# Kernel optimization log

Measured on AMD Instinct MI355X. Metric: run time of the kernel, lower is better.

The kernel has to match this reference:

```python
import jax, jax.numpy as jnp
import numpy as np

B, DIM, H, W = 4, 512, 64, 64
HEADS = 8
MAX_FREQ = 10000.0


def _rope_cos_sin(h, w, head_dim, dtype):
    # 2D RoPE: first quarter of half_dim uses row position, second quarter uses col position
    half = head_dim // 2
    quarter = half // 2
    pos_h = jnp.arange(h, dtype=dtype)
    pos_w = jnp.arange(w, dtype=dtype)
    gh, gw = jnp.meshgrid(pos_h, pos_w, indexing='ij')
    pos = jnp.stack([gh.ravel(), gw.ravel()], axis=-1)  # [N, 2]
    freqs = 1.0 / (MAX_FREQ ** (jnp.arange(quarter, dtype=dtype) / quarter))  # [quarter]
    ang_x = pos[:, 0:1] * freqs  # [N, quarter]
    ang_y = pos[:, 1:2] * freqs  # [N, quarter]
    cos = jnp.concatenate([jnp.cos(ang_x), jnp.cos(ang_y)], axis=-1)  # [N, half]
    sin = jnp.concatenate([jnp.sin(ang_x), jnp.sin(ang_y)], axis=-1)  # [N, half]
    return cos, sin


def _apply_rope(x, cos, sin):
    # x: [B, heads, N, head_dim]; cos/sin: [N, head_dim//2]
    d = x.shape[-1] // 2
    x1, x2 = x[..., :d], x[..., d:]
    return jnp.concatenate([x1 * cos - x2 * sin, x1 * sin + x2 * cos], axis=-1)


def setup_inputs() -> dict:
    key = jax.random.key(0)
    kx, kq, kp = jax.random.split(key, 3)
    x = jax.random.normal(kx, (B, DIM, H, W), dtype=jnp.float32)
    w_qkv = jax.random.normal(kq, (3 * DIM, DIM), dtype=jnp.float32) * (DIM ** -0.5)
    w_proj = jax.random.normal(kp, (DIM, DIM), dtype=jnp.float32) * (DIM ** -0.5)
    return {"x": x, "w_qkv": w_qkv, "w_proj": w_proj}


def reference(x, w_qkv, w_proj):
    Bb, C, Hh, Ww = x.shape
    heads = HEADS
    hd = C // heads
    N = Hh * Ww
    # 1x1 conv (bias-free) == channel-wise linear
    qkv = jnp.einsum('bchw,oc->bohw', x, w_qkv)  # [B, 3C, H, W]
    qkv = qkv.reshape(Bb, 3, heads, hd, Hh, Ww).transpose(1, 0, 2, 4, 5, 3)  # [3, B, heads, H, W, hd]
    q = qkv[0].reshape(Bb, heads, N, hd)
    k = qkv[1].reshape(Bb, heads, N, hd)
    v = qkv[2].reshape(Bb, heads, N, hd)
    cos, sin = _rope_cos_sin(Hh, Ww, hd, x.dtype)
    q = _apply_rope(q, cos, sin)
    k = _apply_rope(k, cos, sin)
    scale = hd ** -0.5
    attn = jax.nn.softmax(jnp.einsum('bhnd,bhmd->bhnm', q, k) * scale, axis=-1)  # [B, heads, N, N]
    out = jnp.einsum('bhnm,bhmd->bhnd', attn, v)  # [B, heads, N, hd]
    out = out.reshape(Bb, heads, Hh, Ww, hd).transpose(0, 1, 4, 2, 3).reshape(Bb, C, Hh, Ww)
    return jnp.einsum('bchw,oc->bohw', out, w_proj)
```

## Files before the change

### kernel.cpp

```cpp
#include <hip/hip_runtime.h>
#include <math.h>

#define B_    4
#define CDIM  512
#define HEADS 8
#define HD    64
#define NN    4096
#define QSZ   ((size_t)B_*HEADS*NN*HD)
#define SCALE_Q 0.18033688011112042f

typedef __attribute__((ext_vector_type(8))) short short8;
typedef __attribute__((ext_vector_type(4))) float f32x4;
typedef __attribute__((ext_vector_type(16))) float f32x16;
union U4S8 { uint4 u; short8 s; };

__device__ inline unsigned pk(float a, float b) {
    unsigned ua = __float_as_uint(a), ub = __float_as_uint(b);
    ua += 0x7FFFu + ((ua >> 16) & 1u);
    ub += 0x7FFFu + ((ub >> 16) & 1u);
    return (ua >> 16) | (ub & 0xFFFF0000u);
}
__device__ inline unsigned short bf16_1(float a) {
    unsigned ua = __float_as_uint(a);
    ua += 0x7FFFu + ((ua >> 16) & 1u);
    return (unsigned short)(ua >> 16);
}
__device__ inline unsigned cvtpk(float a, float b) {
    unsigned r;
    asm("v_cvt_pk_bf16_f32 %0, %1, %2" : "=v"(r) : "v"(a), "v"(b));
    return r;
}

__device__ inline void load_lds16(const unsigned short* g, unsigned short* l) {
    __builtin_amdgcn_global_load_lds(
        (const __attribute__((address_space(1))) unsigned int*)g,
        (__attribute__((address_space(3))) unsigned int*)l, 16, 0, 0);
}

__global__ void conv_w_kernel(const float* __restrict__ wq, const float* __restrict__ wp,
                              unsigned short* __restrict__ wqb, unsigned short* __restrict__ wpb) {
    int id = blockIdx.x * 256 + threadIdx.x;
    const float* src; unsigned short* dst; size_t off; float sc = 1.0f;
    if (id < 98304) { src = wq; dst = wqb; off = (size_t)id * 8; if (off < 262144) sc = SCALE_Q; }
    else            { src = wp; dst = wpb; off = (size_t)(id - 98304) * 8; }
    float4 a = *(const float4*)(src + off);
    float4 b = *(const float4*)(src + off + 4);
    uint4 u;
    u.x = pk(a.x * sc, a.y * sc); u.y = pk(a.z * sc, a.w * sc);
    u.z = pk(b.x * sc, b.y * sc); u.w = pk(b.z * sc, b.w * sc);
    *(uint4*)(dst + off) = u;
}

__global__ void rope_table_kernel(float* __restrict__ ct, float* __restrict__ st) {
    int id = blockIdx.x * 256 + threadIdx.x;
    int j = id >> 12, n = id & 4095;
    int i = j & 15;
    float pos = (j < 16) ? (float)(n >> 6) : (float)(n & 63);
    float freq = exp2f(-(float)i * 0.8304820237218406f);
    float ang = pos * freq;
    ct[id] = cosf(ang);
    st[id] = sinf(ang);
}

__global__ __launch_bounds__(256) void transpose_x_kernel(
        const float* __restrict__ x, unsigned short* __restrict__ xt) {
    __shared__ unsigned short T[64 * 72];
    int t = threadIdx.x;
    int b = blockIdx.z, c0 = blockIdx.y * 64, n0 = blockIdx.x * 64;
    const float* xb = x + ((size_t)b * CDIM + c0) * NN + n0;
    int crow = t >> 2, nseg = t & 3;
#pragma unroll
    for (int g = 0; g < 4; ++g) {
        float4 f = *(const float4*)(xb + (size_t)crow * NN + nseg * 16 + g * 4);
        int nb = nseg * 16 + g * 4;
        T[(nb + 0) * 72 + crow] = bf16_1(f.x);
        T[(nb + 1) * 72 + crow] = bf16_1(f.y);
        T[(nb + 2) * 72 + crow] = bf16_1(f.z);
        T[(nb + 3) * 72 + crow] = bf16_1(f.w);
    }
    __syncthreads();
    unsigned short* xo = xt + ((size_t)b * NN + n0) * CDIM + c0;
    int nrow = t >> 2, cseg = t & 3;
    uint4 u0 = *(uint4*)(T + nrow * 72 + cseg * 16);
    uint4 u1 = *(uint4*)(T + nrow * 72 + cseg * 16 + 8);
    *(uint4*)(xo + (size_t)nrow * CDIM + cseg * 16)     = u0;
    *(uint4*)(xo + (size_t)nrow * CDIM + cseg * 16 + 8) = u1;
}

__global__ __launch_bounds__(256, 2) void qkv_mfma_kernel(
        const unsigned short* __restrict__ xt, const unsigned short* __restrict__ wq,
        unsigned short* __restrict__ qbf, unsigned short* __restrict__ kbf,
        unsigned short* __restrict__ vt,
        const float* __restrict__ ct, const float* __restrict__ st) {
    __shared__ unsigned short smem[8192];
    int t = threadIdx.x;
    int lane = t & 63, w = t >> 6;
    int qlo = lane & 15, quad = lane >> 4;
    int b = blockIdx.z, o0 = blockIdx.y * 128, n0 = blockIdx.x * 128;
    const unsigned short* xb = xt + (size_t)b * NN * CDIM;
    int row = t >> 2, seg = t & 3;
    int wn = (w & 1) * 64, wo = (w >> 1) * 64;

    f32x4 acc[4][4];
#pragma unroll
    for (int i = 0; i < 4; ++i)
#pragma unroll
        for (int j = 0; j < 4; ++j) acc[i][j] = f32x4{0.f, 0.f, 0.f, 0.f};

    for (int k0 = 0; k0 < 512; k0 += 32) {
        __syncthreads();
        load_lds16(xb + (size_t)(n0 + row) * 512 + k0 + seg * 8,        smem + t * 8);
        load_lds16(xb + (size_t)(n0 + 64 + row) * 512 + k0 + seg * 8,   smem + 2048 + t * 8);
        load_lds16(wq + (size_t)(o0 + row) * 512 + k0 + seg * 8,        smem + 4096 + t * 8);
        load_lds16(wq + (size_t)(o0 + 64 + row) * 512 + k0 + seg * 8,   smem + 6144 + t * 8);
        __syncthreads();
        U4S8 af[4], bf[4];
#pragma unroll
        for (int mt = 0; mt < 4; ++mt)
            af[mt].u = *(const uint4*)(smem + (wn + 16 * mt + qlo) * 32 + quad * 8);
#pragma unroll
        for (int nt = 0; nt < 4; ++nt)
            bf[nt].u = *(const uint4*)(smem + 4096 + (wo + 16 * nt + qlo) * 32 + quad * 8);
#pragma unroll
        for (int mt = 0; mt < 4; ++mt)
#pragma unroll
            for (int nt = 0; nt < 4; ++nt)
                acc[mt][nt] = __builtin_amdgcn_mfma_f32_16x16x32_bf16(
                    af[mt].s, bf[nt].s, acc[mt][nt], 0, 0, 0);
    }

    int og = o0 + wo;
    int s = og >> 9;
    int h = (og & 511) >> 6;
    int bh = b * HEADS + h;
    if (s < 2) {
        unsigned short* dst = (s ? kbf : qbf) + (size_t)bh * NN * HD;
#pragma unroll
        for (int mt = 0; mt < 4; ++mt) {
            int nbase = n0 + wn + 16 * mt + 4 * quad;
#pragma unroll
            for (int ntp = 0; ntp < 2; ++ntp) {
                int j = 16 * ntp + qlo;
                float4 c4 = *(const float4*)(ct + (size_t)j * NN + nbase);
                float4 s4 = *(const float4*)(st + (size_t)j * NN + nbase);
                float cc[4] = {c4.x, c4.y, c4.z, c4.w};
                float ss[4] = {s4.x, s4.y, s4.z, s4.w};
#pragma unroll
                for (int r = 0; r < 4; ++r) {
                    float x1 = acc[mt][ntp][r], x2 = acc[mt][ntp + 2][r];
                    size_t base = (size_t)(nbase + r) * HD;
                    dst[base + j]      = bf16_1(x1 * cc[r] - x2 * ss[r]);
                    dst[base + j + 32] = bf16_1(x1 * ss[r] + x2 * cc[r]);
                }
            }
        }
    } else {
        unsigned short* dst = vt + (size_t)bh * HD * NN;
#pragma unroll
        for (int mt = 0; mt < 4; ++mt)
#pragma unroll
            for (int nt = 0; nt < 4; ++nt) {
                int d = 16 * nt + qlo;
                int n = n0 + wn + 16 * mt + 4 * quad;
                uint2 u;
                u.x = pk(acc[mt][nt][0], acc[mt][nt][1]);
                u.y = pk(acc[mt][nt][2], acc[mt][nt][3]);
                *(uint2*)(dst + (size_t)d * NN + n) = u;
            }
    }
}

#define EXP_GRP(Sv, MTQ, KSL, PA)                                        \
    {                                                                    \
        float p0 = __builtin_amdgcn_exp2f(Sv[8 * (KSL) + 0]);            \
        float p1 = __builtin_amdgcn_exp2f(Sv[8 * (KSL) + 1]);            \
        float p2 = __builtin_amdgcn_exp2f(Sv[8 * (KSL) + 2]);            \
        float p3 = __builtin_amdgcn_exp2f(Sv[8 * (KSL) + 3]);            \
        float p4 = __builtin_amdgcn_exp2f(Sv[8 * (KSL) + 4]);            \
        float p5 = __builtin_amdgcn_exp2f(Sv[8 * (KSL) + 5]);            \
        float p6 = __builtin_amdgcn_exp2f(Sv[8 * (KSL) + 6]);            \
        float p7 = __builtin_amdgcn_exp2f(Sv[8 * (KSL) + 7]);            \
        Lsum[MTQ] += ((p0 + p1) + (p2 + p3)) + ((p4 + p5) + (p6 + p7));  \
        PA.u.x = cvtpk(p0, p1); PA.u.y = cvtpk(p2, p3);                  \
        PA.u.z = cvtpk(p4, p5); PA.u.w = cvtpk(p6, p7);                  \
    }

#define MFMA32(A, B, C) __builtin_amdgcn_mfma_f32_32x32x16_bf16((A), (B), (C), 0, 0, 0)

#define HALF_STEP_PF(SCONS, SPROD, KAC, KAN, KN_B, KN_H, VB_B, V_H)                      \
    {                                                                                    \
        U4S8 vb0, vb1, vb2, vb3;                                                         \
        vb0.u = *(const uint4*)((VB_B) + l31 * 144 + (V_H) * 64 + 16 * h);               \
        vb1.u = *(const uint4*)((VB_B) + (32 + l31) * 144 + (V_H) * 64 + 16 * h);        \
        vb2.u = *(const uint4*)((VB_B) + l31 * 144 + (V_H) * 64 + 32 + 16 * h);          \
        vb3.u = *(const uint4*)((VB_B) + (32 + l31) * 144 + (V_H) * 64 + 32 + 16 * h);   \
        KAN[0].u = *(const uint4*)((KN_B) + ((KN_H) * 32 + l31) * 144 + 16 * h);         \
        KAN[1].u = *(const uint4*)((KN_B) + ((KN_H) * 32 + l31) * 144 + 32 + 16 * h);    \
        KAN[2].u = *(const uint4*)((KN_B) + ((KN_H) * 32 + l31) * 144 + 64 + 16 * h);    \
        KAN[3].u = *(const uint4*)((KN_B) + ((KN_H) * 32 + l31) * 144 + 96 + 16 * h);    \
        U4S8 pa[2][2];                                                                   \
        SPROD[0] = MFMA32(KAC[0].s, qf[0][0].s, Zv);                                     \
        SPROD[1] = MFMA32(KAC[0].s, qf[1][0].s, Zv);                                     \
        EXP_GRP(SCONS[0], 0, 0, pa[0][0]);                                               \
        SPROD[0] = MFMA32(KAC[1].s, qf[0][1].s, SPROD[0]);                               \
        SPROD[1] = MFMA32(KAC[1].s, qf[1][1].s, SPROD[1]);                               \
        EXP_GRP(SCONS[0], 0, 1, pa[1][0]);                                               \
        SPROD[0] = MFMA32(KAC[2].s, qf[0][2].s, SPROD[0]);                               \
        SPROD[1] = MFMA32(KAC[2].s, qf[1][2].s, SPROD[1]);                               \
        EXP_GRP(SCONS[1], 1, 0, pa[0][1]);                                               \
        SPROD[0] = MFMA32(KAC[3].s, qf[0][3].s, SPROD[0]);                               \
        SPROD[1] = MFMA32(KAC[3].s, qf[1][3].s, SPROD[1]);                               \
        EXP_GRP(SCONS[1], 1, 1, pa[1][1]);                                               \
        O[0][0] = MFMA32(pa[0][0].s, vb0.s, O[0][0]);                                    \
        O[1][0] = MFMA32(pa[0][1].s, vb0.s, O[1][0]);                                    \
        O[0][1] = MFMA32(pa[0][0].s, vb1.s, O[0][1]);                                    \
        O[1][1] = MFMA32(pa[0][1].s, vb1.s, O[1][1]);                                    \
        O[0][0] = MFMA32(pa[1][0].s, vb2.s, O[0][0]);                                    \
        O[1][0] = MFMA32(pa[1][1].s, vb2.s, O[1][0]);                                    \
        O[0][1] = MFMA32(pa[1][0].s, vb3.s, O[0][1]);                                    \
        O[1][1] = MFMA32(pa[1][1].s, vb3.s, O[1][1]);                                    \
    }

__global__ __launch_bounds__(256, 2) void attn_kernel(
        const unsigned short* __restrict__ qbf, const unsigned short* __restrict__ kbf,
        const unsigned short* __restrict__ vt, unsigned short* __restrict__ aot) {
    __shared__ unsigned char smem[55296];
    int t = threadIdx.x;
    int lane = t & 63, w = t >> 6;
    int l31 = lane & 31, h = lane >> 5;
    int bb = blockIdx.z, hh = blockIdx.y;
    int bh = bb * HEADS + hh;
    int n0w = blockIdx.x * 256 + w * 64;

    U4S8 qf[2][4];
    const unsigned short* qg = qbf + ((size_t)bh * NN + n0w) * HD;
#pragma unroll
    for (int mtq = 0; mtq < 2; ++mtq)
#pragma unroll
        for (int ks = 0; ks < 4; ++ks)
            qf[mtq][ks].u = *(const uint4*)(qg + (size_t)(32 * mtq + l31) * 64 + 16 * ks + 8 * h);

    f32x16 Zv;
#pragma unroll
    for (int i = 0; i < 16; ++i) Zv[i] = 0.f;

    f32x16 O[2][2];
#pragma unroll
    for (int mtq = 0; mtq < 2; ++mtq)
#pragma unroll
        for (int ntd = 0; ntd < 2; ++ntd) O[mtq][ntd] = Zv;
    float Lsum[2] = {0.f, 0.f};

    const uint4* kg = (const uint4*)kbf + (size_t)bh * NN * 8;
    const uint4* vg = (const uint4*)vt  + (size_t)bh * 64 * 512;

    int rr0 = t >> 3, s8 = t & 7;
    int voff = 32 * (s8 >> 1) + 8 * (s8 & 1);

    const uint4* kp0 = kg + rr0 * 8 + s8;
    const uint4* kp1 = kg + (32 + rr0) * 8 + s8;
    const uint4* vp0 = vg + rr0 * 512 + s8;
    const uint4* vp1 = vg + (32 + rr0) * 512 + s8;

    unsigned char* kd0 = smem + rr0 * 144 + s8 * 16;
    unsigned char* kd1 = smem + (32 + rr0) * 144 + s8 * 16;
    unsigned char* vd0 = smem + 9216 + rr0 * 144 + voff;
    unsigned char* vd1 = smem + 9216 + (32 + rr0) * 144 + voff;

    uint4 kr0, kr1, vr0, vr1;
#pragma unroll
    for (int pt = 0; pt < 2; ++pt) {
        kr0 = kp0[0]; kr1 = kp1[0]; vr0 = vp0[0]; vr1 = vp1[0];
        kp0 += 512; kp1 += 512; vp0 += 8; vp1 += 8;
        int bo = pt * 18432;
        *(uint4*)(kd0 + bo) = kr0;
        *(uint4*)(kd1 + bo) = kr1;
        *(uint2*)(vd0 + bo)      = make_uint2(vr0.x, vr0.y);
        *(uint2*)(vd0 + bo + 16) = make_uint2(vr0.z, vr0.w);
        *(uint2*)(vd1 + bo)      = make_uint2(vr1.x, vr1.y);
        *(uint2*)(vd1 + bo + 16) = make_uint2(vr1.z, vr1.w);
    }
    kr0 = kp0[0]; kr1 = kp1[0]; vr0 = vp0[0]; vr1 = vp1[0];
    kp0 += 512; kp1 += 512; vp0 += 8; vp1 += 8;
    __syncthreads();

    f32x16 SA[2], SB[2];
    U4S8 kaA[4], kaB[4];
    {
        U4S8 ka0, ka1, ka2, ka3;
        ka0.u = *(const uint4*)(smem + l31 * 144 + 16 * h);
        ka1.u = *(const uint4*)(smem + l31 * 144 + 32 + 16 * h);
        ka2.u = *(const uint4*)(smem + l31 * 144 + 64 + 16 * h);
        ka3.u = *(const uint4*)(smem + l31 * 144 + 96 + 16 * h);
        kaA[0].u = *(const uint4*)(smem + (32 + l31) * 144 + 16 * h);
        kaA[1].u = *(const uint4*)(smem + (32 + l31) * 144 + 32 + 16 * h);
        kaA[2].u = *(const uint4*)(smem + (32 + l31) * 144 + 64 + 16 * h);
        kaA[3].u = *(const uint4*)(smem + (32 + l31) * 144 + 96 + 16 * h);
        SB[0] = MFMA32(ka0.s, qf[0][0].s, Zv);
        SB[1] = MFMA32(ka0.s, qf[1][0].s, Zv);
        SB[0] = MFMA32(ka1.s, qf[0][1].s, SB[0]);
        SB[1] = MFMA32(ka1.s, qf[1][1].s, SB[1]);
        SB[0] = MFMA32(ka2.s, qf[0][2].s, SB[0]);
        SB[1] = MFMA32(ka2.s, qf[1][2].s, SB[1]);
        SB[0] = MFMA32(ka3.s, qf[0][3].s, SB[0]);
        SB[1] = MFMA32(ka3.s, qf[1][3].s, SB[1]);
    }

    int b0 = 0, b1 = 18432, b2 = 36864;
    for (int c = 0; c < 63; ++c) {
        *(uint4*)(kd0 + b2) = kr0;
        *(uint4*)(kd1 + b2) = kr1;
        *(uint2*)(vd0 + b2)      = make_uint2(vr0.x, vr0.y);
        *(uint2*)(vd0 + b2 + 16) = make_uint2(vr0.z, vr0.w);
        *(uint2*)(vd1 + b2)      = make_uint2(vr1.x, vr1.y);
        *(uint2*)(vd1 + b2 + 16) = make_uint2(vr1.z, vr1.w);
        kr0 = kp0[0]; kr1 = kp1[0]; vr0 = vp0[0]; vr1 = vp1[0];
        kp0 += 512; kp1 += 512; vp0 += 8; vp1 += 8;

        __builtin_amdgcn_s_setprio(1);
        HALF_STEP_PF(SB, SA, kaA, kaB, smem + b1, 0, smem + b0 + 9216, 0)
        HALF_STEP_PF(SA, SB, kaB, kaA, smem + b1, 1, smem + b0 + 9216, 1)
        __builtin_amdgcn_s_setprio(0);

        int tmp = b0; b0 = b1; b1 = b2; b2 = tmp;
        __syncthreads();
    }

    {
        U4S8 vb0, vb1, vb2, vb3;
        const unsigned char* vbb = smem + b0 + 9216;
        vb0.u = *(const uint4*)(vbb + l31 * 144 + 16 * h);
        vb1.u = *(const uint4*)(vbb + (32 + l31) * 144 + 16 * h);
        vb2.u = *(const uint4*)(vbb + l31 * 144 + 32 + 16 * h);
        vb3.u = *(const uint4*)(vbb + (32 + l31) * 144 + 32 + 16 * h);
        U4S8 pa[2][2];
        SA[0] = MFMA32(kaA[0].s, qf[0][0].s, Zv);
        SA[1] = MFMA32(kaA[0].s, qf[1][0].s, Zv);
        EXP_GRP(SB[0], 0, 0, pa[0][0]);
        SA[0] = MFMA32(kaA[1].s, qf[0][1].s, SA[0]);
        SA[1] = MFMA32(kaA[1].s, qf[1][1].s, SA[1]);
        EXP_GRP(SB[0], 0, 1, pa[1][0]);
        SA[0] = MFMA32(kaA[2].s, qf[0][2].s, SA[0]);
        SA[1] = MFMA32(kaA[2].s, qf[1][2].s, SA[1]);
        EXP_GRP(SB[1], 1, 0, pa[0][1]);
        SA[0] = MFMA32(kaA[3].s, qf[0][3].s, SA[0]);
        SA[1] = MFMA32(kaA[3].s, qf[1][3].s, SA[1]);
        EXP_GRP(SB[1], 1, 1, pa[1][1]);
        O[0][0] = MFMA32(pa[0][0].s, vb0.s, O[0][0]);
        O[1][0] = MFMA32(pa[0][1].s, vb0.s, O[1][0]);
        O[0][1] = MFMA32(pa[0][0].s, vb1.s, O[0][1]);
        O[1][1] = MFMA32(pa[0][1].s, vb1.s, O[1][1]);
        O[0][0] = MFMA32(pa[1][0].s, vb2.s, O[0][0]);
        O[1][0] = MFMA32(pa[1][1].s, vb2.s, O[1][0]);
        O[0][1] = MFMA32(pa[1][0].s, vb3.s, O[0][1]);
        O[1][1] = MFMA32(pa[1][1].s, vb3.s, O[1][1]);
    }
    {
        U4S8 pa[2][2];
        EXP_GRP(SA[0], 0, 0, pa[0][0]);
        EXP_GRP(SA[0], 0, 1, pa[1][0]);
        EXP_GRP(SA[1], 1, 0, pa[0][1]);
        EXP_GRP(SA[1], 1, 1, pa[1][1]);
        const unsigned char* vbb = smem + b0 + 9216;
        { U4S8 vb; vb.u = *(const uint4*)(vbb + l31 * 144 + 64 + 16 * h);
          O[0][0] = MFMA32(pa[0][0].s, vb.s, O[0][0]);
          O[1][0] = MFMA32(pa[0][1].s, vb.s, O[1][0]); }
        { U4S8 vb; vb.u = *(const uint4*)(vbb + (32 + l31) * 144 + 64 + 16 * h);
          O[0][1] = MFMA32(pa[0][0].s, vb.s, O[0][1]);
          O[1][1] = MFMA32(pa[0][1].s, vb.s, O[1][1]); }
        { U4S8 vb; vb.u = *(const uint4*)(vbb + l31 * 144 + 96 + 16 * h);
          O[0][0] = MFMA32(pa[1][0].s, vb.s, O[0][0]);
          O[1][0] = MFMA32(pa[1][1].s, vb.s, O[1][0]); }
        { U4S8 vb; vb.u = *(const uint4*)(vbb + (32 + l31) * 144 + 96 + 16 * h);
          O[0][1] = MFMA32(pa[1][0].s, vb.s, O[0][1]);
          O[1][1] = MFMA32(pa[1][1].s, vb.s, O[1][1]); }
    }

    float Linv[2];
#pragma unroll
    for (int mtq = 0; mtq < 2; ++mtq) {
        float l = Lsum[mtq] + __shfl_xor(Lsum[mtq], 32, 64);
        Linv[mtq] = 1.0f / l;
    }
    __syncthreads();
    unsigned short* Tw = (unsigned short*)(smem + w * 4608);
    unsigned short* aob = aot + ((size_t)bb * NN) * CDIM + hh * 64;
#pragma unroll
    for (int mtq = 0; mtq < 2; ++mtq) {
        float iv[16];
#pragma unroll
        for (int r = 0; r < 16; ++r) {
            int src = (r & 3) + 8 * ((r >> 2) & 1) + 16 * (r >> 3) + 4 * h;
            iv[r] = __shfl(Linv[mtq], src, 64);
        }
#pragma unroll
        for (int rg = 0; rg < 2; ++rg) {
#pragma unroll
            for (int ntd = 0; ntd < 2; ++ntd)
#pragma unroll
                for (int rr = 0; rr < 8; ++rr) {
                    int r = 8 * rg + rr;
                    int q16 = (rr & 3) + 8 * (rr >> 2) + 4 * h;
                    Tw[q16 * 72 + 32 * ntd + l31] = bf16_1(O[mtq][ntd][r] * iv[r]);
                }
            int row = lane >> 2, cseg = lane & 3;
            uint4 u0 = *(uint4*)(Tw + row * 72 + cseg * 16);
            uint4 u1 = *(uint4*)(Tw + row * 72 + cseg * 16 + 8);
            unsigned short* arow = aob
                + (size_t)(n0w + 32 * mtq + 16 * rg + row) * CDIM + cseg * 16;
            *(uint4*)(arow)     = u0;
            *(uint4*)(arow + 8) = u1;
        }
    }
}

__global__ __launch_bounds__(256, 2) void proj_mfma_kernel(
        const unsigned short* __restrict__ aot, const unsigned short* __restrict__ wp,
        float* __restrict__ out) {
    __shared__ unsigned short smem[8192];
    int t = threadIdx.x;
    int lane = t & 63, w = t >> 6;
    int qlo = lane & 15, quad = lane >> 4;
    int b = blockIdx.z, o0 = blockIdx.y * 128, n0 = blockIdx.x * 128;
    const unsigned short* ab = aot + (size_t)b * NN * CDIM;
    int row = t >> 2, seg = t & 3;
    int wn = (w & 1) * 64, wo = (w >> 1) * 64;

    f32x4 acc[4][4];
#pragma unroll
    for (int i = 0; i < 4; ++i)
#pragma unroll
        for (int j = 0; j < 4; ++j) acc[i][j] = f32x4{0.f, 0.f, 0.f, 0.f};

    for (int k0 = 0; k0 < 512; k0 += 32) {
        __syncthreads();
        load_lds16(ab + (size_t)(n0 + row) * 512 + k0 + seg * 8,        smem + t * 8);
        load_lds16(ab + (size_t)(n0 + 64 + row) * 512 + k0 + seg * 8,   smem + 2048 + t * 8);
        load_lds16(wp + (size_t)(o0 + row) * 512 + k0 + seg * 8,        smem + 4096 + t * 8);
        load_lds16(wp + (size_t)(o0 + 64 + row) * 512 + k0 + seg * 8,   smem + 6144 + t * 8);
        __syncthreads();
        U4S8 af[4], bf[4];
#pragma unroll
        for (int mt = 0; mt < 4; ++mt)
            af[mt].u = *(const uint4*)(smem + (wn + 16 * mt + qlo) * 32 + quad * 8);
#pragma unroll
        for (int nt = 0; nt < 4; ++nt)
            bf[nt].u = *(const uint4*)(smem + 4096 + (wo + 16 * nt + qlo) * 32 + quad * 8);
#pragma unroll
        for (int mt = 0; mt < 4; ++mt)
#pragma unroll
            for (int nt = 0; nt < 4; ++nt)
                acc[mt][nt] = __builtin_amdgcn_mfma_f32_16x16x32_bf16(
                    af[mt].s, bf[nt].s, acc[mt][nt], 0, 0, 0);
    }

    float* ob = out + (size_t)b * CDIM * NN;
#pragma unroll
    for (int mt = 0; mt < 4; ++mt)
#pragma unroll
        for (int nt = 0; nt < 4; ++nt) {
            int o = o0 + wo + 16 * nt + qlo;
            int n = n0 + wn + 16 * mt + 4 * quad;
            *(float4*)(ob + (size_t)o * NN + n) = *(float4*)&acc[mt][nt];
        }
}

extern "C" void kernel_launch(void* const* d_in, const int* in_sizes, int n_in,
                              void* d_out, int out_size, void* d_ws, size_t ws_size,
                              hipStream_t stream) {
    const float* x      = (const float*)d_in[0];
    const float* w_qkv  = (const float*)d_in[1];
    const float* w_proj = (const float*)d_in[2];
    float* out = (float*)d_out;
    unsigned short* ws = (unsigned short*)d_ws;

    unsigned short* xt  = ws;
    unsigned short* qbf = xt  + QSZ;
    unsigned short* kbf = qbf + QSZ;
    unsigned short* vt  = kbf + QSZ;
    unsigned short* aot = vt  + QSZ;
    unsigned short* wqb = aot + QSZ;
    unsigned short* wpb = wqb + 786432;
    float* ct = (float*)(wpb + 262144);
    float* st = ct + 32 * 4096;

    conv_w_kernel<<<512, 256, 0, stream>>>(w_qkv, w_proj, wqb, wpb);
    rope_table_kernel<<<512, 256, 0, stream>>>(ct, st);
    transpose_x_kernel<<<dim3(64, 8, B_), 256, 0, stream>>>(x, xt);
    qkv_mfma_kernel<<<dim3(32, 12, B_), 256, 0, stream>>>(xt, wqb, qbf, kbf, vt, ct, st);
    attn_kernel<<<dim3(NN / 256, HEADS, B_), 256, 0, stream>>>(qbf, kbf, vt, aot);
    proj_mfma_kernel<<<dim3(32, 4, B_), 256, 0, stream>>>(aot, wpb, out);
}
```

Before: 279.0 us.

## Double-buffer QKV and projection GEMM LDS tiles with XOR swizzle and 64-wide K

```diff
diff --git a/kernel.cpp b/kernel.cpp
--- a/kernel.cpp
+++ b/kernel.cpp
@@ -87,18 +87,56 @@
     *(uint4*)(xo + (size_t)nrow * CDIM + cseg * 16 + 8) = u1;
 }
 
+#define GEMM_STAGE(SRC_A, SRC_B, ST, K0)                                               \
+    {                                                                                  \
+        unsigned short* sdst = smem + (ST) * 16384;                                    \
+        _Pragma("unroll")                                                              \
+        for (int i = 0; i < 4; ++i) {                                                  \
+            int R  = 32 * i + row;                                                     \
+            int sg = (seg ^ (R & 7)) * 8;                                              \
+            load_lds16((SRC_A) + (size_t)(n0 + R) * 512 + (K0) + sg,                   \
+                       sdst + i * 2048 + t * 8);                                       \
+            load_lds16((SRC_B) + (size_t)(o0 + R) * 512 + (K0) + sg,                   \
+                       sdst + 8192 + i * 2048 + t * 8);                                \
+        }                                                                              \
+    }
+
+#define GEMM_KSTEP(SB)                                                                 \
+    _Pragma("unroll")                                                                  \
+    for (int kk = 0; kk < 2; ++kk) {                                                   \
+        U4S8 af[4], bf4[4];                                                            \
+        _Pragma("unroll")                                                              \
+        for (int mt = 0; mt < 4; ++mt) {                                               \
+            int R = wn + 16 * mt + qlo;                                                \
+            af[mt].u = *(const uint4*)((SB) + R * 64 +                                 \
+                        ((kk * 32 + quad * 8) ^ ((R & 7) * 8)));                       \
+        }                                                                              \
+        _Pragma("unroll")                                                              \
+        for (int nt = 0; nt < 4; ++nt) {                                               \
+            int R = wo + 16 * nt + qlo;                                                \
+            bf4[nt].u = *(const uint4*)((SB) + 8192 + R * 64 +                         \
+                        ((kk * 32 + quad * 8) ^ ((R & 7) * 8)));                       \
+        }                                                                              \
+        _Pragma("unroll")                                                              \
+        for (int mt = 0; mt < 4; ++mt)                                                 \
+            _Pragma("unroll")                                                          \
+            for (int nt = 0; nt < 4; ++nt)                                             \
+                acc[mt][nt] = __builtin_amdgcn_mfma_f32_16x16x32_bf16(                 \
+                    af[mt].s, bf4[nt].s, acc[mt][nt], 0, 0, 0);                        \
+    }
+
 __global__ __launch_bounds__(256, 2) void qkv_mfma_kernel(
         const unsigned short* __restrict__ xt, const unsigned short* __restrict__ wq,
         unsigned short* __restrict__ qbf, unsigned short* __restrict__ kbf,
         unsigned short* __restrict__ vt,
         const float* __restrict__ ct, const float* __restrict__ st) {
-    __shared__ unsigned short smem[8192];
+    __shared__ unsigned short smem[32768];
     int t = threadIdx.x;
     int lane = t & 63, w = t >> 6;
     int qlo = lane & 15, quad = lane >> 4;
     int b = blockIdx.z, o0 = blockIdx.y * 128, n0 = blockIdx.x * 128;
     const unsigned short* xb = xt + (size_t)b * NN * CDIM;
-    int row = t >> 2, seg = t & 3;
+    int row = t >> 3, seg = t & 7;
     int wn = (w & 1) * 64, wo = (w >> 1) * 64;
 
     f32x4 acc[4][4];
@@ -107,26 +145,12 @@
 #pragma unroll
         for (int j = 0; j < 4; ++j) acc[i][j] = f32x4{0.f, 0.f, 0.f, 0.f};
 
-    for (int k0 = 0; k0 < 512; k0 += 32) {
+    GEMM_STAGE(xb, wq, 0, 0)
+    for (int it = 0; it < 8; ++it) {
         __syncthreads();
-        load_lds16(xb + (size_t)(n0 + row) * 512 + k0 + seg * 8,        smem + t * 8);
-        load_lds16(xb + (size_t)(n0 + 64 + row) * 512 + k0 + seg * 8,   smem + 2048 + t * 8);
-        load_lds16(wq + (size_t)(o0 + row) * 512 + k0 + seg * 8,        smem + 4096 + t * 8);
-        load_lds16(wq + (size_t)(o0 + 64 + row) * 512 + k0 + seg * 8,   smem + 6144 + t * 8);
-        __syncthreads();
-        U4S8 af[4], bf[4];
-#pragma unroll
-        for (int mt = 0; mt < 4; ++mt)
-            af[mt].u = *(const uint4*)(smem + (wn + 16 * mt + qlo) * 32 + quad * 8);
-#pragma unroll
-        for (int nt = 0; nt < 4; ++nt)
-            bf[nt].u = *(const uint4*)(smem + 4096 + (wo + 16 * nt + qlo) * 32 + quad * 8);
-#pragma unroll
-        for (int mt = 0; mt < 4; ++mt)
-#pragma unroll
-            for (int nt = 0; nt < 4; ++nt)
-                acc[mt][nt] = __builtin_amdgcn_mfma_f32_16x16x32_bf16(
-                    af[mt].s, bf[nt].s, acc[mt][nt], 0, 0, 0);
+        if (it < 7) GEMM_STAGE(xb, wq, (it + 1) & 1, (it + 1) * 64)
+        const unsigned short* s = smem + (it & 1) * 16384;
+        GEMM_KSTEP(s)
     }
 
     int og = o0 + wo;
@@ -417,13 +441,13 @@
 __global__ __launch_bounds__(256, 2) void proj_mfma_kernel(
         const unsigned short* __restrict__ aot, const unsigned short* __restrict__ wp,
         float* __restrict__ out) {
-    __shared__ unsigned short smem[8192];
+    __shared__ unsigned short smem[32768];
     int t = threadIdx.x;
     int lane = t & 63, w = t >> 6;
     int qlo = lane & 15, quad = lane >> 4;
     int b = blockIdx.z, o0 = blockIdx.y * 128, n0 = blockIdx.x * 128;
     const unsigned short* ab = aot + (size_t)b * NN * CDIM;
-    int row = t >> 2, seg = t & 3;
+    int row = t >> 3, seg = t & 7;
     int wn = (w & 1) * 64, wo = (w >> 1) * 64;
 
     f32x4 acc[4][4];
@@ -432,26 +456,12 @@
 #pragma unroll
         for (int j = 0; j < 4; ++j) acc[i][j] = f32x4{0.f, 0.f, 0.f, 0.f};
 
-    for (int k0 = 0; k0 < 512; k0 += 32) {
+    GEMM_STAGE(ab, wp, 0, 0)
+    for (int it = 0; it < 8; ++it) {
         __syncthreads();
-        load_lds16(ab + (size_t)(n0 + row) * 512 + k0 + seg * 8,        smem + t * 8);
-        load_lds16(ab + (size_t)(n0 + 64 + row) * 512 + k0 + seg * 8,   smem + 2048 + t * 8);
-        load_lds16(wp + (size_t)(o0 + row) * 512 + k0 + seg * 8,        smem + 4096 + t * 8);
-        load_lds16(wp + (size_t)(o0 + 64 + row) * 512 + k0 + seg * 8,   smem + 6144 + t * 8);
-        __syncthreads();
-        U4S8 af[4], bf[4];
-#pragma unroll
-        for (int mt = 0; mt < 4; ++mt)
-            af[mt].u = *(const uint4*)(smem + (wn + 16 * mt + qlo) * 32 + quad * 8);
-#pragma unroll
-        for (int nt = 0; nt < 4; ++nt)
-            bf[nt].u = *(const uint4*)(smem + 4096 + (wo + 16 * nt + qlo) * 32 + quad * 8);
-#pragma unroll
-        for (int mt = 0; mt < 4; ++mt)
-#pragma unroll
-            for (int nt = 0; nt < 4; ++nt)
-                acc[mt][nt] = __builtin_amdgcn_mfma_f32_16x16x32_bf16(
-                    af[mt].s, bf[nt].s, acc[mt][nt], 0, 0, 0);
+        if (it < 7) GEMM_STAGE(ab, wp, (it + 1) & 1, (it + 1) * 64)
+        const unsigned short* s = smem + (it & 1) * 16384;
+        GEMM_KSTEP(s)
     }
 
     float* ob = out + (size_t)b * CDIM * NN;
```

Measured after the change: 280.7 us. Within noise of the previous version (+0.6%).
